# Optimization experiments

Hardware: AMD Instinct MI355X
Metric: run time of the kernel (lower is better)

The kernel has to match this reference:

```python
import jax, jax.numpy as jnp
import numpy as np

H, D = 16, 1024
HD = D // H  # 64

def setup_inputs() -> dict:
    key = jax.random.key(0)
    ks = jax.random.split(key, 11)
    B, S = 2, 2048
    s_in = 1.0 / np.sqrt(D)
    return {
        "V": jax.random.normal(ks[0], (B, S, D), jnp.float32),
        "K": jax.random.normal(ks[1], (B, S, D), jnp.float32),
        "Q": jax.random.normal(ks[2], (B, S, D), jnp.float32),
        # stacked per-head Linear weights, torch layout [out,in] -> [H, HD, D]
        "Wv": jax.random.normal(ks[3], (H, HD, D), jnp.float32) * s_in,
        "bv": jnp.zeros((H, HD), jnp.float32),
        "Wk": jax.random.normal(ks[4], (H, HD, D), jnp.float32) * s_in,
        "bk": jnp.zeros((H, HD), jnp.float32),
        "Wq": jax.random.normal(ks[5], (H, HD, D), jnp.float32) * s_in,
        "bq": jnp.zeros((H, HD), jnp.float32),
        "Wo": jax.random.normal(ks[6], (D, D), jnp.float32) * s_in,
        "bo": jnp.zeros((D,), jnp.float32),
    }

def reference(V, K, Q, Wv, bv, Wk, bk, Wq, bq, Wo, bo):
    scale = HD ** (-0.5)
    # per-head projections fused into one batched GEMM: [B,S,D] x [H,HD,D] -> [B,H,S,HD]
    q = jnp.einsum('bsd,hed->bhse', Q, Wq) + bq[None, :, None, :]
    k = jnp.einsum('bsd,hed->bhse', K, Wk) + bk[None, :, None, :]
    v = jnp.einsum('bsd,hed->bhse', V, Wv) + bv[None, :, None, :]
    # scaled dot-product attention
    scores = jnp.einsum('bhqe,bhke->bhqk', q, k) * scale  # [B,H,S,S]
    p = jax.nn.softmax(scores, axis=-1)
    att = jnp.einsum('bhqk,bhke->bhqe', p, v)  # [B,H,S,HD]
    # concat heads (head 0 first, matching the torch cat order) then output proj
    B, _, S, _ = att.shape
    cat = jnp.transpose(att, (0, 2, 1, 3)).reshape(B, S, H * HD)
    return cat @ Wo.T + bo
```

## Files before the change

kernel.cpp:

```cpp
#include <hip/hip_runtime.h>
#include <cstdint>
#include <cstddef>

typedef __bf16 bf16_t;
typedef bf16_t bf16x8 __attribute__((ext_vector_type(8)));
typedef bf16_t bf16x4 __attribute__((ext_vector_type(4)));
typedef float f32x4 __attribute__((ext_vector_type(4)));

__device__ __forceinline__ void gl_lds16(const void* g, void* l) {
  __builtin_amdgcn_global_load_lds(
      (const __attribute__((address_space(1))) void*)g,
      (__attribute__((address_space(3))) void*)l, 16, 0, 0);
}

__device__ __forceinline__ f32x4 mfma16(bf16x8 a, bf16x8 b, f32x4 c) {
  return __builtin_amdgcn_mfma_f32_16x16x32_bf16(a, b, c, 0, 0, 0);
}

struct CvtWArgs { const float* src[4]; };

__global__ __launch_bounds__(256) void convert_w(CvtWArgs a, bf16_t* __restrict__ dst) {
  unsigned g = blockIdx.x * 256u + threadIdx.x;
  unsigned seg = g >> 17, off = g & 0x1FFFFu;
  const float4* s = (const float4*)a.src[seg] + (size_t)off * 2;
  float4 x0 = s[0], x1 = s[1];
  bf16x8 o;
  o[0] = (bf16_t)x0.x; o[1] = (bf16_t)x0.y; o[2] = (bf16_t)x0.z; o[3] = (bf16_t)x0.w;
  o[4] = (bf16_t)x1.x; o[5] = (bf16_t)x1.y; o[6] = (bf16_t)x1.z; o[7] = (bf16_t)x1.w;
  *(bf16x8*)(dst + (size_t)g * 8) = o;
}

struct ProjArgs {
  const float* A[3]; const bf16_t* W[3]; const float* bias[3];
  bf16_t* out[3]; float scale[3];
};

__global__ __launch_bounds__(256, 5) void gemm_proj(ProjArgs p) {
  __shared__ __attribute__((aligned(16))) unsigned char smem[24576];
  bf16_t* a_s = (bf16_t*)smem;
  bf16_t* b_s = (bf16_t*)(smem + 8192);
  const int K = 1024;
  const int z = blockIdx.z;
  const float*  A = p.A[z] + (size_t)blockIdx.x * 64 * K;
  const bf16_t* W = p.W[z] + (size_t)blockIdx.y * 128 * K;

  const int t = threadIdx.x;
  const int l = t & 63;
  const int lq = l >> 4, lr = l & 15;
  const int w = t >> 6;
  const int mh = w & 1, nh = w >> 1;

  const int ar0 = t >> 4, ac16 = t & 15;
  f32x4 acc[2][4];
  f32x4 zero = {0.f, 0.f, 0.f, 0.f};
  #pragma unroll
  for (int i = 0; i < 2; i++)
    #pragma unroll
    for (int j = 0; j < 4; j++) acc[i][j] = zero;

  for (int kt = 0; kt < 16; ++kt) {
    const int k0 = kt * 64;
    float4 av[4];
    #pragma unroll
    for (int f = 0; f < 4; f++)
      av[f] = *(const float4*)(A + (size_t)(ar0 + f * 16) * K + k0 + ac16 * 4);
    __syncthreads();
    #pragma unroll
    for (int i = 0; i < 4; i++) {
      int g = t + i * 256;
      int r = g >> 3, pc = g & 7;
      int lc = pc ^ (r & 7);
      gl_lds16(W + (size_t)r * K + k0 + lc * 8, b_s + i * 2048 + w * 512);
    }
    #pragma unroll
    for (int f = 0; f < 4; f++) {
      int r = ar0 + f * 16;
      int phys = (ac16 >> 1) ^ (r & 7);
      bf16x4 bv;
      bv[0] = (bf16_t)av[f].x; bv[1] = (bf16_t)av[f].y;
      bv[2] = (bf16_t)av[f].z; bv[3] = (bf16_t)av[f].w;
      *(bf16x4*)(a_s + r * 64 + phys * 8 + (ac16 & 1) * 4) = bv;
    }
    __syncthreads();
    #pragma unroll
    for (int kk = 0; kk < 2; kk++) {
      bf16x8 af[2], bfr[4];
      #pragma unroll
      for (int i = 0; i < 2; i++) {
        int R = mh * 32 + i * 16 + lr;
        int ch = (kk * 4 + lq) ^ (R & 7);
        af[i] = *(const bf16x8*)(a_s + R * 64 + ch * 8);
      }
      #pragma unroll
      for (int j = 0; j < 4; j++) {
        int R = nh * 64 + j * 16 + lr;
        int ch = (kk * 4 + lq) ^ (R & 7);
        bfr[j] = *(const bf16x8*)(b_s + R * 64 + ch * 8);
      }
      #pragma unroll
      for (int i = 0; i < 2; i++)
        #pragma unroll
        for (int j = 0; j < 4; j++)
          acc[i][j] = mfma16(af[i], bfr[j], acc[i][j]);
    }
  }

  const float* bias = p.bias[z];
  const float scale = p.scale[z];
  __syncthreads();
  const int b = blockIdx.x >> 5;
  const int sbase = (blockIdx.x & 31) * 64;
  bf16_t* out = p.out[z];
  if (z == 0) {
    bf16_t* ts = (bf16_t*)smem;
    #pragma unroll
    for (int i = 0; i < 2; i++) {
      #pragma unroll
      for (int j = 0; j < 4; j++) {
        int nl = nh * 64 + j * 16 + lr;
        float bz = bias[blockIdx.y * 128 + nl];
        #pragma unroll
        for (int r = 0; r < 4; r++) {
          int ml = mh * 32 + i * 16 + lq * 4 + r;
          int mlp = (ml & 32) | (((ml >> 2) & 3) << 3) |
                    (((ml >> 4) & 1) << 2) | (ml & 3);
          ts[nl * 72 + mlp] = (bf16_t)((acc[i][j][r] + bz) * scale);
        }
      }
    }
    __syncthreads();
    #pragma unroll
    for (int ii = 0; ii < 4; ii++) {
      int idx = t * 8 + ii * 2048;
      int rr = idx >> 6, cc = idx & 63;
      int n = blockIdx.y * 128 + rr;
      int h = n >> 6, e = n & 63;
      bf16x8 vq = *(const bf16x8*)(ts + rr * 72 + cc);
      *(bf16x8*)(out + ((size_t)(b * 16 + h) * 64 + e) * 2048 + sbase + cc) = vq;
    }
  } else {
    bf16_t* ts = (bf16_t*)smem;
    #pragma unroll
    for (int i = 0; i < 2; i++) {
      #pragma unroll
      for (int j = 0; j < 4; j++) {
        int nl = nh * 64 + j * 16 + lr;
        float bz = bias[blockIdx.y * 128 + nl];
        #pragma unroll
        for (int r = 0; r < 4; r++) {
          int ml = mh * 32 + i * 16 + lq * 4 + r;
          ts[ml * 136 + nl] = (bf16_t)((acc[i][j][r] + bz) * scale);
        }
      }
    }
    __syncthreads();
    #pragma unroll
    for (int ii = 0; ii < 4; ii++) {
      int idx = t * 8 + ii * 2048;
      int rr = idx >> 7, cc = idx & 127;
      int n = blockIdx.y * 128 + cc;
      int h = n >> 6, e = n & 63;
      bf16x8 vq = *(const bf16x8*)(ts + rr * 136 + cc);
      *(bf16x8*)(out + ((size_t)(b * 16 + h) * 2048 + sbase + rr) * 64 + e) = vq;
    }
  }
}

__global__ __launch_bounds__(256, 4) void attn(
    const bf16_t* __restrict__ qw, const bf16_t* __restrict__ kw,
    const bf16_t* __restrict__ vtw, bf16_t* __restrict__ att)
{
  __shared__ bf16_t k_s[64 * 64];
  __shared__ bf16_t v_s[64 * 64];
  __shared__ bf16_t qe_s[64 * 72];
  const int bh = blockIdx.x, qt = blockIdx.y;
  const int t = threadIdx.x, w = t >> 6, l = t & 63, lq = l >> 4, lr = l & 15;

  const bf16_t* qbase = qw + ((size_t)bh * 2048 + qt * 64) * 64;
  #pragma unroll
  for (int i = 0; i < 2; i++) {
    int g = t + i * 256;
    int r = g >> 3, pc = g & 7;
    int lc = pc ^ (r & 7);
    gl_lds16(qbase + (size_t)r * 64 + lc * 8, qe_s + i * 2048 + w * 512);
  }
  __syncthreads();
  bf16x8 qf[2];
  #pragma unroll
  for (int kk = 0; kk < 2; kk++) {
    int R = w * 16 + lr;
    int ch = (kk * 4 + lq) ^ (R & 7);
    qf[kk] = *(const bf16x8*)(qe_s + R * 64 + ch * 8);
  }

  f32x4 O[4];
  f32x4 zero = {0.f, 0.f, 0.f, 0.f};
  #pragma unroll
  for (int et = 0; et < 4; et++) O[et] = zero;
  float lsum = 0.f;

  for (int kt = 0; kt < 32; ++kt) {
    __syncthreads();
    const bf16_t* kbase = kw + ((size_t)bh * 2048 + kt * 64) * 64;
    const bf16_t* vbase = vtw + (size_t)bh * 131072 + (size_t)kt * 64;
    #pragma unroll
    for (int i = 0; i < 2; i++) {
      int g = t + i * 256;
      int r = g >> 3, pc = g & 7;
      int lc = pc ^ (r & 7);
      gl_lds16(kbase + (size_t)r * 64 + lc * 8, k_s + i * 2048 + w * 512);
      gl_lds16(vbase + (size_t)r * 2048 + lc * 8, v_s + i * 2048 + w * 512);
    }
    __syncthreads();

    f32x4 sc[4];
    #pragma unroll
    for (int j = 0; j < 4; j++) sc[j] = zero;
    #pragma unroll
    for (int kk = 0; kk < 2; kk++) {
      #pragma unroll
      for (int j = 0; j < 4; j++) {
        int R = j * 16 + lr;
        int ch = (kk * 4 + lq) ^ (R & 7);
        bf16x8 kf = *(const bf16x8*)(k_s + R * 64 + ch * 8);
        sc[j] = mfma16(kf, qf[kk], sc[j]);
      }
    }

    bf16x8 pb[2];
    #pragma unroll
    for (int ks2 = 0; ks2 < 2; ks2++) {
      #pragma unroll
      for (int r = 0; r < 4; r++) {
        float e0 = __expf(sc[2 * ks2][r]);
        float e1 = __expf(sc[2 * ks2 + 1][r]);
        lsum += e0 + e1;
        pb[ks2][r] = (bf16_t)e0;
        pb[ks2][4 + r] = (bf16_t)e1;
      }
    }

    #pragma unroll
    for (int ks2 = 0; ks2 < 2; ks2++) {
      #pragma unroll
      for (int et = 0; et < 4; et++) {
        int R = et * 16 + lr;
        int ch = (ks2 * 4 + lq) ^ (R & 7);
        bf16x8 vf = *(const bf16x8*)(v_s + R * 64 + ch * 8);
        O[et] = mfma16(vf, pb[ks2], O[et]);
      }
    }
  }

  float s = lsum;
  s += __shfl_xor(s, 16);
  s += __shfl_xor(s, 32);
  float rinv = 1.0f / s;

  #pragma unroll
  for (int et = 0; et < 4; et++) {
    bf16x4 pv;
    #pragma unroll
    for (int r = 0; r < 4; r++) pv[r] = (bf16_t)(O[et][r] * rinv);
    *(bf16x4*)(qe_s + (w * 16 + lr) * 72 + et * 16 + lq * 4) = pv;
  }
  __syncthreads();
  const int b = bh >> 4, h = bh & 15;
  #pragma unroll
  for (int i = 0; i < 2; i++) {
    int c = t + i * 256;
    int row = c >> 3, c8 = c & 7;
    bf16x8 vv = *(const bf16x8*)(qe_s + row * 72 + c8 * 8);
    *(bf16x8*)(att + ((size_t)b * 2048 + qt * 64 + row) * 1024 + h * 64 + c8 * 8) = vv;
  }
}

__global__ __launch_bounds__(256, 4) void gemm_out(
    const bf16_t* __restrict__ A, const bf16_t* __restrict__ W,
    const float* __restrict__ bias, float* __restrict__ out)
{
  __shared__ bf16_t a_s[64 * 64];
  __shared__ bf16_t b_s[64 * 64];
  const int K = 1024;
  const bf16_t* Ab = A + (size_t)blockIdx.x * 64 * K;
  const bf16_t* Wb = W + (size_t)blockIdx.y * 64 * K;
  const int t = threadIdx.x, w = t >> 6, l = t & 63, lq = l >> 4, lr = l & 15;
  const int mh = w & 1, nh = w >> 1;

  f32x4 acc[2][2];
  f32x4 zero = {0.f, 0.f, 0.f, 0.f};
  #pragma unroll
  for (int i = 0; i < 2; i++)
    #pragma unroll
    for (int j = 0; j < 2; j++) acc[i][j] = zero;

  for (int k0 = 0; k0 < K; k0 += 64) {
    __syncthreads();
    #pragma unroll
    for (int i = 0; i < 2; i++) {
      int g = t + i * 256;
      int r = g >> 3, pc = g & 7;
      int lc = pc ^ (r & 7);
      gl_lds16(Ab + (size_t)r * K + k0 + lc * 8, a_s + i * 2048 + w * 512);
      gl_lds16(Wb + (size_t)r * K + k0 + lc * 8, b_s + i * 2048 + w * 512);
    }
    __syncthreads();
    #pragma unroll
    for (int kk = 0; kk < 2; kk++) {
      bf16x8 af[2], bfr[2];
      #pragma unroll
      for (int i = 0; i < 2; i++) {
        int R = mh * 32 + i * 16 + lr;
        int ch = (kk * 4 + lq) ^ (R & 7);
        af[i] = *(const bf16x8*)(a_s + R * 64 + ch * 8);
      }
      #pragma unroll
      for (int j = 0; j < 2; j++) {
        int R = nh * 32 + j * 16 + lr;
        int ch = (kk * 4 + lq) ^ (R & 7);
        bfr[j] = *(const bf16x8*)(b_s + R * 64 + ch * 8);
      }
      #pragma unroll
      for (int i = 0; i < 2; i++)
        #pragma unroll
        for (int j = 0; j < 2; j++)
          acc[i][j] = mfma16(af[i], bfr[j], acc[i][j]);
    }
  }

  #pragma unroll
  for (int i = 0; i < 2; i++) {
    #pragma unroll
    for (int j = 0; j < 2; j++) {
      int col = blockIdx.y * 64 + nh * 32 + j * 16 + lr;
      float bz = bias[col];
      #pragma unroll
      for (int r = 0; r < 4; r++) {
        int row = blockIdx.x * 64 + mh * 32 + i * 16 + lq * 4 + r;
        out[(size_t)row * 1024 + col] = acc[i][j][r] + bz;
      }
    }
  }
}

extern "C" void kernel_launch(void* const* d_in, const int* in_sizes, int n_in,
                              void* d_out, int out_size, void* d_ws, size_t ws_size,
                              hipStream_t stream) {
  (void)in_sizes; (void)n_in; (void)out_size;
  const float* V  = (const float*)d_in[0];
  const float* Kx = (const float*)d_in[1];
  const float* Q  = (const float*)d_in[2];
  const float* Wv = (const float*)d_in[3];
  const float* bv = (const float*)d_in[4];
  const float* Wk = (const float*)d_in[5];
  const float* bk = (const float*)d_in[6];
  const float* Wq = (const float*)d_in[7];
  const float* bq = (const float*)d_in[8];
  const float* Wo = (const float*)d_in[9];
  const float* bo = (const float*)d_in[10];

  const size_t E = 1048576;
  if (ws_size < 20 * E * sizeof(bf16_t)) return;

  bf16_t* ws = (bf16_t*)d_ws;
  bf16_t* cWo   = ws;
  bf16_t* cWv   = ws + E;
  bf16_t* cWk   = ws + 2 * E;
  bf16_t* cWq   = ws + 3 * E;
  bf16_t* q_ws  = ws + 4 * E;
  bf16_t* k_ws  = ws + 8 * E;
  bf16_t* vt_ws = ws + 12 * E;
  bf16_t* att_ws= ws + 16 * E;

  CvtWArgs cw;
  cw.src[0] = Wo; cw.src[1] = Wv; cw.src[2] = Wk; cw.src[3] = Wq;
  convert_w<<<2048, 256, 0, stream>>>(cw, ws);

  ProjArgs pa;
  pa.A[0] = V;   pa.A[1] = Kx;  pa.A[2] = Q;
  pa.W[0] = cWv; pa.W[1] = cWk; pa.W[2] = cWq;
  pa.bias[0] = bv; pa.bias[1] = bk; pa.bias[2] = bq;
  pa.out[0] = vt_ws; pa.out[1] = k_ws; pa.out[2] = q_ws;
  pa.scale[0] = 1.f; pa.scale[1] = 1.f; pa.scale[2] = 0.125f;
  gemm_proj<<<dim3(64, 8, 3), 256, 0, stream>>>(pa);

  attn<<<dim3(32, 32), 256, 0, stream>>>(q_ws, k_ws, vt_ws, att_ws);

  gemm_out<<<dim3(64, 16), 256, 0, stream>>>(att_ws, cWo, bo, (float*)d_out);
}
```

Measured before the change: 216.2 us.

## Register-prefetch next tiles and use lighter barriers in projection, attention, output GEMM

Replaces direct global-to-LDS loads with register-staged prefetch: the next K-tile is loaded into registers while the current tile is computed, then written to LDS at the top of the next iteration. Full __syncthreads barriers are replaced with custom s_barrier sequences that wait only on LDS counters, so outstanding global prefetches can stay in flight across the barrier. This aims to hide global memory latency behind MFMA work in all three kernels. It costs extra VGPRs, which could cut occupancy, and the hand-written barriers rely on the compiler inserting vmcnt waits before the register stores.

```diff
diff --git a/kernel.cpp b/kernel.cpp
--- a/kernel.cpp
+++ b/kernel.cpp
@@ -15,6 +15,13 @@
 
 __device__ __forceinline__ f32x4 mfma16(bf16x8 a, bf16x8 b, f32x4 c) {
   return __builtin_amdgcn_mfma_f32_16x16x32_bf16(a, b, c, 0, 0, 0);
+}
+
+__device__ __forceinline__ void bar_sync() {
+  asm volatile("s_barrier" ::: "memory");
+}
+__device__ __forceinline__ void bar_publish() {
+  asm volatile("s_waitcnt lgkmcnt(0)\n\ts_barrier" ::: "memory");
 }
 
 struct CvtWArgs { const float* src[4]; };
@@ -58,20 +65,17 @@
     #pragma unroll
     for (int j = 0; j < 4; j++) acc[i][j] = zero;
 
+  float4 av[4]; uint4 wv[4];
+  #pragma unroll
+  for (int f = 0; f < 4; f++)
+    av[f] = *(const float4*)(A + (size_t)(ar0 + f * 16) * K + ac16 * 4);
+  #pragma unroll
+  for (int i = 0; i < 4; i++) {
+    int g = t + i * 256, r = g >> 3, pc = g & 7, lc = pc ^ (r & 7);
+    wv[i] = *(const uint4*)(W + (size_t)r * K + lc * 8);
+  }
+
   for (int kt = 0; kt < 16; ++kt) {
-    const int k0 = kt * 64;
-    float4 av[4];
-    #pragma unroll
-    for (int f = 0; f < 4; f++)
-      av[f] = *(const float4*)(A + (size_t)(ar0 + f * 16) * K + k0 + ac16 * 4);
-    __syncthreads();
-    #pragma unroll
-    for (int i = 0; i < 4; i++) {
-      int g = t + i * 256;
-      int r = g >> 3, pc = g & 7;
-      int lc = pc ^ (r & 7);
-      gl_lds16(W + (size_t)r * K + k0 + lc * 8, b_s + i * 2048 + w * 512);
-    }
     #pragma unroll
     for (int f = 0; f < 4; f++) {
       int r = ar0 + f * 16;
@@ -81,7 +85,21 @@
       bv[2] = (bf16_t)av[f].z; bv[3] = (bf16_t)av[f].w;
       *(bf16x4*)(a_s + r * 64 + phys * 8 + (ac16 & 1) * 4) = bv;
     }
-    __syncthreads();
+    #pragma unroll
+    for (int i = 0; i < 4; i++)
+      *(uint4*)(b_s + (t + i * 256) * 8) = wv[i];
+    if (kt < 15) {
+      const int k0 = (kt + 1) * 64;
+      #pragma unroll
+      for (int f = 0; f < 4; f++)
+        av[f] = *(const float4*)(A + (size_t)(ar0 + f * 16) * K + k0 + ac16 * 4);
+      #pragma unroll
+      for (int i = 0; i < 4; i++) {
+        int g = t + i * 256, r = g >> 3, pc = g & 7, lc = pc ^ (r & 7);
+        wv[i] = *(const uint4*)(W + (size_t)r * K + k0 + lc * 8);
+      }
+    }
+    bar_publish();
     #pragma unroll
     for (int kk = 0; kk < 2; kk++) {
       bf16x8 af[2], bfr[4];
@@ -103,11 +121,11 @@
         for (int j = 0; j < 4; j++)
           acc[i][j] = mfma16(af[i], bfr[j], acc[i][j]);
     }
+    bar_sync();
   }
 
   const float* bias = p.bias[z];
   const float scale = p.scale[z];
-  __syncthreads();
   const int b = blockIdx.x >> 5;
   const int sbase = (blockIdx.x & 31) * 64;
   bf16_t* out = p.out[z];
@@ -128,7 +146,7 @@
         }
       }
     }
-    __syncthreads();
+    bar_publish();
     #pragma unroll
     for (int ii = 0; ii < 4; ii++) {
       int idx = t * 8 + ii * 2048;
@@ -153,7 +171,7 @@
         }
       }
     }
-    __syncthreads();
+    bar_publish();
     #pragma unroll
     for (int ii = 0; ii < 4; ii++) {
       int idx = t * 8 + ii * 2048;
@@ -199,19 +217,34 @@
   for (int et = 0; et < 4; et++) O[et] = zero;
   float lsum = 0.f;
 
+  const bf16_t* kb0 = kw + (size_t)bh * 131072;
+  const bf16_t* vb0 = vtw + (size_t)bh * 131072;
+  uint4 kv[2], vv[2];
+  #pragma unroll
+  for (int i = 0; i < 2; i++) {
+    int g = t + i * 256, r = g >> 3, pc = g & 7, lc = pc ^ (r & 7);
+    kv[i] = *(const uint4*)(kb0 + r * 64 + lc * 8);
+    vv[i] = *(const uint4*)(vb0 + (size_t)r * 2048 + lc * 8);
+  }
+
   for (int kt = 0; kt < 32; ++kt) {
-    __syncthreads();
-    const bf16_t* kbase = kw + ((size_t)bh * 2048 + kt * 64) * 64;
-    const bf16_t* vbase = vtw + (size_t)bh * 131072 + (size_t)kt * 64;
     #pragma unroll
     for (int i = 0; i < 2; i++) {
       int g = t + i * 256;
-      int r = g >> 3, pc = g & 7;
-      int lc = pc ^ (r & 7);
-      gl_lds16(kbase + (size_t)r * 64 + lc * 8, k_s + i * 2048 + w * 512);
-      gl_lds16(vbase + (size_t)r * 2048 + lc * 8, v_s + i * 2048 + w * 512);
-    }
-    __syncthreads();
+      *(uint4*)(k_s + g * 8) = kv[i];
+      *(uint4*)(v_s + g * 8) = vv[i];
+    }
+    if (kt < 31) {
+      const bf16_t* kb = kb0 + (kt + 1) * 4096;
+      const bf16_t* vb = vb0 + (kt + 1) * 64;
+      #pragma unroll
+      for (int i = 0; i < 2; i++) {
+        int g = t + i * 256, r = g >> 3, pc = g & 7, lc = pc ^ (r & 7);
+        kv[i] = *(const uint4*)(kb + r * 64 + lc * 8);
+        vv[i] = *(const uint4*)(vb + (size_t)r * 2048 + lc * 8);
+      }
+    }
+    bar_publish();
 
     f32x4 sc[4];
     #pragma unroll
@@ -250,6 +283,7 @@
         O[et] = mfma16(vf, pb[ks2], O[et]);
       }
     }
+    bar_sync();
   }
 
   float s = lsum;
@@ -264,14 +298,14 @@
     for (int r = 0; r < 4; r++) pv[r] = (bf16_t)(O[et][r] * rinv);
     *(bf16x4*)(qe_s + (w * 16 + lr) * 72 + et * 16 + lq * 4) = pv;
   }
-  __syncthreads();
+  bar_publish();
   const int b = bh >> 4, h = bh & 15;
   #pragma unroll
   for (int i = 0; i < 2; i++) {
     int c = t + i * 256;
     int row = c >> 3, c8 = c & 7;
-    bf16x8 vv = *(const bf16x8*)(qe_s + row * 72 + c8 * 8);
-    *(bf16x8*)(att + ((size_t)b * 2048 + qt * 64 + row) * 1024 + h * 64 + c8 * 8) = vv;
+    bf16x8 vv2 = *(const bf16x8*)(qe_s + row * 72 + c8 * 8);
+    *(bf16x8*)(att + ((size_t)b * 2048 + qt * 64 + row) * 1024 + h * 64 + c8 * 8) = vv2;
   }
 }
 
@@ -294,17 +328,31 @@
     #pragma unroll
     for (int j = 0; j < 2; j++) acc[i][j] = zero;
 
-  for (int k0 = 0; k0 < K; k0 += 64) {
-    __syncthreads();
+  uint4 avv[2], wv[2];
+  #pragma unroll
+  for (int i = 0; i < 2; i++) {
+    int g = t + i * 256, r = g >> 3, pc = g & 7, lc = pc ^ (r & 7);
+    avv[i] = *(const uint4*)(Ab + (size_t)r * K + lc * 8);
+    wv[i]  = *(const uint4*)(Wb + (size_t)r * K + lc * 8);
+  }
+
+  for (int kt = 0; kt < 16; ++kt) {
     #pragma unroll
     for (int i = 0; i < 2; i++) {
       int g = t + i * 256;
-      int r = g >> 3, pc = g & 7;
-      int lc = pc ^ (r & 7);
-      gl_lds16(Ab + (size_t)r * K + k0 + lc * 8, a_s + i * 2048 + w * 512);
-      gl_lds16(Wb + (size_t)r * K + k0 + lc * 8, b_s + i * 2048 + w * 512);
-    }
-    __syncthreads();
+      *(uint4*)(a_s + g * 8) = avv[i];
+      *(uint4*)(b_s + g * 8) = wv[i];
+    }
+    if (kt < 15) {
+      const int k0 = (kt + 1) * 64;
+      #pragma unroll
+      for (int i = 0; i < 2; i++) {
+        int g = t + i * 256, r = g >> 3, pc = g & 7, lc = pc ^ (r & 7);
+        avv[i] = *(const uint4*)(Ab + (size_t)r * K + k0 + lc * 8);
+        wv[i]  = *(const uint4*)(Wb + (size_t)r * K + k0 + lc * 8);
+      }
+    }
+    bar_publish();
     #pragma unroll
     for (int kk = 0; kk < 2; kk++) {
       bf16x8 af[2], bfr[2];
@@ -326,6 +374,7 @@
         for (int j = 0; j < 2; j++)
           acc[i][j] = mfma16(af[i], bfr[j], acc[i][j]);
     }
+    bar_sync();
   }
 
   #pragma unroll
```

New measurement: 439.4 us. +103.3%, slower.
